# Kernel optimization log

Hardware: AMD Instinct MI355X
Metric: run time of the kernel (lower is better)

Reference implementation:

```python
import jax, jax.numpy as jnp
import numpy as np

N = 50000      # nodes
E = 1600000    # edges
IN = 128       # in_feats
H = 4          # heads
F = 32         # per-head feats (h_feats = out_feats = 32)
NEG_SLOPE = 0.2


def setup_inputs() -> dict:
    key = jax.random.key(0)
    ks = jax.random.split(key, 12)
    glorot = lambda k, shape: jax.random.normal(k, shape, jnp.float32) * np.sqrt(2.0 / (shape[0] + shape[-1])).astype(np.float32)
    x = jax.random.normal(ks[0], (N, IN), jnp.float32)
    edge_index = jax.random.randint(ks[1], (2, E), 0, N, dtype=jnp.int32)
    W1 = glorot(ks[2], (IN, H * F))
    att_src1 = glorot(ks[3], (H, F))
    att_dst1 = glorot(ks[4], (H, F))
    b1 = jnp.zeros((F,), jnp.float32)
    W2 = glorot(ks[5], (F, H * F))
    att_src2 = glorot(ks[6], (H, F))
    att_dst2 = glorot(ks[7], (H, F))
    b2 = jnp.zeros((F,), jnp.float32)
    return {"x": x, "edge_index": edge_index,
            "W1": W1, "att_src1": att_src1, "att_dst1": att_dst1, "b1": b1,
            "W2": W2, "att_src2": att_src2, "att_dst2": att_dst2, "b2": b2}


def gat_conv(x, edge_index, W, a_src, a_dst, bias):
    """PyG GATConv with concat=False (head-average), add_self_loops=True."""
    n = x.shape[0]
    h = (x @ W).reshape(n, H, F)                      # [N,H,F]
    loops = jnp.arange(n, dtype=edge_index.dtype)
    src = jnp.concatenate([edge_index[0], loops])     # [E+N]
    dst = jnp.concatenate([edge_index[1], loops])
    alpha_src = jnp.einsum('nhf,hf->nh', h, a_src)    # [N,H]
    alpha_dst = jnp.einsum('nhf,hf->nh', h, a_dst)
    e = jax.nn.leaky_relu(alpha_src[src] + alpha_dst[dst], NEG_SLOPE)  # [E+N,H]
    # scatter-softmax over incoming edges per destination node
    m = jax.ops.segment_max(e, dst, num_segments=n)
    e = jnp.exp(e - m[dst])
    s = jax.ops.segment_sum(e, dst, num_segments=n)
    alpha = e / (s[dst] + 1e-16)                      # [E+N,H]
    out = jax.ops.segment_sum(alpha[:, :, None] * h[src], dst, num_segments=n)  # [N,H,F]
    return out.mean(axis=1) + bias                    # concat=False: average heads


def reference(x, edge_index, W1, att_src1, att_dst1, b1, W2, att_src2, att_dst2, b2):
    h = gat_conv(x, edge_index, W1, att_src1, att_dst1, b1)
    h = jax.nn.elu(h)
    return gat_conv(h, edge_index, W2, att_src2, att_dst2, b2)
```

## Files before the change

### kernel.cpp

```cpp
#include <hip/hip_runtime.h>
#include <hip/hip_bf16.h>
#include <hip/hip_fp16.h>
#include <math.h>


#define NS 64
#define NB 4
#define MAXNPB 12500

__device__ __forceinline__ float lrelu(float x) { return x > 0.f ? x : 0.2f * x; }

__device__ __forceinline__ unsigned int fenc(float f) {
    unsigned int u = __float_as_uint(f);
    return (u & 0x80000000u) ? ~u : (u | 0x80000000u);
}
__device__ __forceinline__ float fdec(unsigned int e) {
    unsigned int u = (e & 0x80000000u) ? (e & 0x7FFFFFFFu) : ~e;
    return __uint_as_float(u);
}

__device__ __forceinline__ unsigned short f2bf(float x) {
    unsigned u = __float_as_uint(x);
    return (unsigned short)((u + 0x7FFFu + ((u >> 16) & 1u)) >> 16);
}
__device__ __forceinline__ float bflo(unsigned w) { return __uint_as_float(w << 16); }
__device__ __forceinline__ float bfhi(unsigned w) { return __uint_as_float(w & 0xFFFF0000u); }

__device__ __forceinline__ unsigned pack_h2(float a, float b) {
    const __half2 h = __float22half2_rn(make_float2(a, b));
    return *(const unsigned*)&h;
}
__device__ __forceinline__ float2 unpack_h2(unsigned w) {
    __half2 h = *(const __half2*)&w;
    return __half22float2(h);
}

__global__ __launch_bounds__(512) void hist_kernel(
    const int* __restrict__ dst, unsigned short* __restrict__ cnt_priv,
    int E, int n, int npb) {
    __shared__ int h[MAXNPB];
    const int b = blockIdx.x & (NB - 1);
    const int s = blockIdx.x / NB;
    const int lo = b * npb;
    const int hi = min(lo + npb, n);
    const int span = hi - lo;
    if (span <= 0) return;
    for (int j = threadIdx.x; j < span; j += 512) h[j] = 0;
    __syncthreads();
    const int E4 = E >> 2;
    const int len4 = (E4 + NS - 1) / NS;
    const int beg4 = s * len4;
    const int end4 = min(beg4 + len4, E4);
    const int4* dst4 = (const int4*)dst;
    for (int i = beg4 + threadIdx.x; i < end4; i += 512) {
        const int4 d = dst4[i];
        if (d.x >= lo && d.x < hi) atomicAdd(&h[d.x - lo], 1);
        if (d.y >= lo && d.y < hi) atomicAdd(&h[d.y - lo], 1);
        if (d.z >= lo && d.z < hi) atomicAdd(&h[d.z - lo], 1);
        if (d.w >= lo && d.w < hi) atomicAdd(&h[d.w - lo], 1);
    }
    if (s == NS - 1) {
        for (int i = (E4 << 2) + threadIdx.x; i < E; i += 512) {
            const int d = dst[i];
            if (d >= lo && d < hi) atomicAdd(&h[d - lo], 1);
        }
    }
    __syncthreads();
    unsigned short* outp = cnt_priv + (size_t)s * n + lo;
    for (int j = threadIdx.x; j < span; j += 512) outp[j] = (unsigned short)h[j];
}

__global__ __launch_bounds__(256) void scan_part(unsigned short* __restrict__ cnt_priv,
                                                 int* __restrict__ deg,
                                                 int* __restrict__ bsum, int n) {
    __shared__ int red[256];
    const int t = threadIdx.x;
    const int node = blockIdx.x * 256 + t;
    int run = 0;
    if (node < n) {
#pragma unroll 4
        for (int s = 0; s < NS; ++s) {
            unsigned short* p = &cnt_priv[(size_t)s * n + node];
            const int c = *p;
            *p = (unsigned short)run;
            run += c;
        }
        deg[node] = run;
    }
    red[t] = (node < n) ? run : 0;
    __syncthreads();
    for (int o = 128; o > 0; o >>= 1) {
        if (t < o) red[t] += red[t + o];
        __syncthreads();
    }
    if (t == 0) bsum[blockIdx.x] = red[0];
}

__global__ __launch_bounds__(256) void scan_mid(const int* __restrict__ bsum,
                                                int* __restrict__ boff, int nb,
                                                int* __restrict__ rowptr, int n) {
    __shared__ int s[256];
    const int t = threadIdx.x;
    const int v = (t < nb) ? bsum[t] : 0;
    s[t] = v;
    __syncthreads();
    for (int o = 1; o < 256; o <<= 1) {
        const int u = (t >= o) ? s[t - o] : 0;
        __syncthreads();
        s[t] += u;
        __syncthreads();
    }
    if (t < nb) boff[t] = s[t] - v;
    if (t == 255) rowptr[n] = s[255];
}

__global__ __launch_bounds__(256) void scan_final(const int* __restrict__ deg,
                                                  const int* __restrict__ boff,
                                                  int* __restrict__ rowptr, int n) {
    __shared__ int s[256];
    const int t = threadIdx.x;
    const int i = blockIdx.x * 256 + t;
    const int v = (i < n) ? deg[i] : 0;
    s[t] = v;
    __syncthreads();
    for (int o = 1; o < 256; o <<= 1) {
        const int u = (t >= o) ? s[t - o] : 0;
        __syncthreads();
        s[t] += u;
        __syncthreads();
    }
    if (i < n) rowptr[i] = boff[blockIdx.x] + s[t] - v;
}

__global__ __launch_bounds__(512) void scatter_kernel(
    const int* __restrict__ src, const int* __restrict__ dst,
    const int* __restrict__ rowptr, const unsigned short* __restrict__ cnt_priv,
    const float* __restrict__ asrc, const float* __restrict__ adst,
    const unsigned int* __restrict__ gmax,
    uint4* __restrict__ esd, int E, int n, int npb) {
    __shared__ int cur[MAXNPB];
    const int b = blockIdx.x & (NB - 1);
    const int s = blockIdx.x / NB;
    const int lo = b * npb;
    const int hi = min(lo + npb, n);
    const int span = hi - lo;
    if (span <= 0) return;
    {
        const unsigned short* cp = cnt_priv + (size_t)s * n + lo;
        const int* rp = rowptr + lo;
        for (int j = threadIdx.x; j < span; j += 512) cur[j] = rp[j] + (int)cp[j];
    }
    __syncthreads();
    const char* aB = (const char*)asrc;
    const char* dB = (const char*)adst;
    const float g0 = fdec(gmax[0]), g1 = fdec(gmax[1]);
    const float g2 = fdec(gmax[2]), g3 = fdec(gmax[3]);

    auto place = [&](int sv, int dv) {
        const int p = atomicAdd(&cur[dv - lo], 1);
        const unsigned s16 = (unsigned)(sv << 4);
        const unsigned d16 = (unsigned)(dv << 4);
        const float4 as = *(const float4*)(aB + s16);
        const float4 ad = *(const float4*)(dB + d16);
        const float q0 = __expf(lrelu(as.x + ad.x) - lrelu(g0 + ad.x));
        const float q1 = __expf(lrelu(as.y + ad.y) - lrelu(g1 + ad.y));
        const float q2 = __expf(lrelu(as.z + ad.z) - lrelu(g2 + ad.z));
        const float q3 = __expf(lrelu(as.w + ad.w) - lrelu(g3 + ad.w));
        esd[p] = make_uint4(s16, d16, pack_h2(q0, q1), pack_h2(q2, q3));
    };

    const int E4 = E >> 2;
    const int len4 = (E4 + NS - 1) / NS;
    const int beg4 = s * len4;
    const int end4 = min(beg4 + len4, E4);
    const int4* dst4 = (const int4*)dst;
    const int4* src4 = (const int4*)src;
    for (int i = beg4 + threadIdx.x; i < end4; i += 512) {
        const int4 d = dst4[i];
        const int4 sv = src4[i];
        if (d.x >= lo && d.x < hi) place(sv.x, d.x);
        if (d.y >= lo && d.y < hi) place(sv.y, d.y);
        if (d.z >= lo && d.z < hi) place(sv.z, d.z);
        if (d.w >= lo && d.w < hi) place(sv.w, d.w);
    }
    if (s == NS - 1) {
        for (int i = (E4 << 2) + threadIdx.x; i < E; i += 512) {
            const int d = dst[i];
            if (d >= lo && d < hi) place(src[i], d);
        }
    }
}

__global__ __launch_bounds__(256) void edge_w_kernel(
    uint4* __restrict__ esd,
    const float* __restrict__ asrc, const float* __restrict__ adst,
    const unsigned int* __restrict__ gmax, int Etot) {
    const char* aB = (const char*)asrc;
    const char* dB = (const char*)adst;
    const float g0 = fdec(gmax[0]), g1 = fdec(gmax[1]);
    const float g2 = fdec(gmax[2]), g3 = fdec(gmax[3]);
    for (int i = blockIdx.x * blockDim.x + threadIdx.x; i < Etot;
         i += gridDim.x * blockDim.x) {
        const unsigned long long sd =
            __builtin_nontemporal_load((const unsigned long long*)&esd[i]);
        const unsigned s16 = (unsigned)sd;
        const unsigned d16 = (unsigned)(sd >> 32);
        const float4 as = *(const float4*)(aB + s16);
        const float4 ad = *(const float4*)(dB + d16);
        const float q0 = __expf(lrelu(as.x + ad.x) - lrelu(g0 + ad.x));
        const float q1 = __expf(lrelu(as.y + ad.y) - lrelu(g1 + ad.y));
        const float q2 = __expf(lrelu(as.z + ad.z) - lrelu(g2 + ad.z));
        const float q3 = __expf(lrelu(as.w + ad.w) - lrelu(g3 + ad.w));
        const unsigned long long rec =
            ((unsigned long long)pack_h2(q2, q3) << 32) | pack_h2(q0, q1);
        __builtin_nontemporal_store(
            rec, (unsigned long long*)((char*)&esd[i] + 8));
    }
}

template <int K>
__global__ __launch_bounds__(256) void gemm_kernel(
    const float* __restrict__ X, const float* __restrict__ W,
    const float* __restrict__ AttS, const float* __restrict__ AttD,
    unsigned short* __restrict__ Hb, float* __restrict__ asrc, float* __restrict__ adst,
    unsigned int* __restrict__ gmax, int n) {
    constexpr int KC = 32;
    __shared__ __align__(16) float Ws[KC * 128];
    __shared__ __align__(16) float Xs[64 * K];
    __shared__ unsigned int smax[4];
    const int tid = threadIdx.x;

    const int r = tid >> 5;
    const int sub = tid & 31;
    const int head = sub >> 3;
    const int pos = ((head & 1) << 1) | (head >> 1);
    const int fc = (sub & 7) * 4;
    const int rowBase = blockIdx.x * 64;

    if (tid < 4) smax[tid] = 0u;
    {
        const float4* X4 = (const float4*)X;
        float4* Xs4 = (float4*)Xs;
        const int K4 = K / 4;
        for (int i = tid; i < 64 * K4; i += 256) {
            int rr = rowBase + i / K4;
            Xs4[i] = (rr < n) ? X4[(size_t)rr * K4 + (i % K4)] : make_float4(0.f, 0.f, 0.f, 0.f);
        }
    }

    float acc[8][4] = {};
    const float4* Ws4 = (const float4*)Ws;
    for (int kt = 0; kt < K; kt += KC) {
        __syncthreads();
        {
            const float4* W4 = (const float4*)(W + kt * 128);
            float4* WsS = (float4*)Ws;
#pragma unroll
            for (int i = 0; i < 4; ++i) WsS[tid + i * 256] = W4[tid + i * 256];
        }
        __syncthreads();
#pragma unroll
        for (int k = 0; k < KC; k += 4) {
            float4 wv[4];
#pragma unroll
            for (int j = 0; j < 4; ++j) wv[j] = Ws4[(k + j) * 32 + sub];
            float4 xv[8];
#pragma unroll
            for (int b = 0; b < 8; ++b)
                xv[b] = *(const float4*)&Xs[(b * 8 + r) * K + kt + k];
#pragma unroll
            for (int b = 0; b < 8; ++b) {
                acc[b][0] = fmaf(xv[b].x, wv[0].x, acc[b][0]);
                acc[b][1] = fmaf(xv[b].x, wv[0].y, acc[b][1]);
                acc[b][2] = fmaf(xv[b].x, wv[0].z, acc[b][2]);
                acc[b][3] = fmaf(xv[b].x, wv[0].w, acc[b][3]);
                acc[b][0] = fmaf(xv[b].y, wv[1].x, acc[b][0]);
                acc[b][1] = fmaf(xv[b].y, wv[1].y, acc[b][1]);
                acc[b][2] = fmaf(xv[b].y, wv[1].z, acc[b][2]);
                acc[b][3] = fmaf(xv[b].y, wv[1].w, acc[b][3]);
                acc[b][0] = fmaf(xv[b].z, wv[2].x, acc[b][0]);
                acc[b][1] = fmaf(xv[b].z, wv[2].y, acc[b][1]);
                acc[b][2] = fmaf(xv[b].z, wv[2].z, acc[b][2]);
                acc[b][3] = fmaf(xv[b].z, wv[2].w, acc[b][3]);
                acc[b][0] = fmaf(xv[b].w, wv[3].x, acc[b][0]);
                acc[b][1] = fmaf(xv[b].w, wv[3].y, acc[b][1]);
                acc[b][2] = fmaf(xv[b].w, wv[3].z, acc[b][2]);
                acc[b][3] = fmaf(xv[b].w, wv[3].w, acc[b][3]);
            }
        }
    }

    float a_s[4], a_d[4];
#pragma unroll
    for (int j = 0; j < 4; ++j) {
        a_s[j] = AttS[head * 32 + fc + j];
        a_d[j] = AttD[head * 32 + fc + j];
    }
#pragma unroll
    for (int b = 0; b < 8; ++b) {
        const int row = rowBase + b * 8 + r;
        const float p0 = __shfl_xor(acc[b][0], 16);
        const float p1 = __shfl_xor(acc[b][1], 16);
        const float p2 = __shfl_xor(acc[b][2], 16);
        const float p3 = __shfl_xor(acc[b][3], 16);
        if (row < n) {
            if (head < 2) {
                char* base = (char*)Hb + (size_t)row * 256 + (unsigned)fc * 8 + head * 4;
                *(unsigned*)(base + 0)  = (unsigned)f2bf(acc[b][0]) | ((unsigned)f2bf(p0) << 16);
                *(unsigned*)(base + 8)  = (unsigned)f2bf(acc[b][1]) | ((unsigned)f2bf(p1) << 16);
                *(unsigned*)(base + 16) = (unsigned)f2bf(acc[b][2]) | ((unsigned)f2bf(p2) << 16);
                *(unsigned*)(base + 24) = (unsigned)f2bf(acc[b][3]) | ((unsigned)f2bf(p3) << 16);
            }
            float ps = acc[b][0] * a_s[0] + acc[b][1] * a_s[1] +
                       acc[b][2] * a_s[2] + acc[b][3] * a_s[3];
            float pd = acc[b][0] * a_d[0] + acc[b][1] * a_d[1] +
                       acc[b][2] * a_d[2] + acc[b][3] * a_d[3];
#pragma unroll
            for (int msk = 1; msk < 8; msk <<= 1) {
                ps += __shfl_xor(ps, msk);
                pd += __shfl_xor(pd, msk);
            }
            if ((sub & 7) == 0) {
                asrc[row * 4 + pos] = ps;
                adst[row * 4 + pos] = pd;
                atomicMax(&smax[pos], fenc(ps));
            }
        }
    }
    __syncthreads();
    if (tid < 4) atomicMax(&gmax[tid], smax[tid]);
}

__global__ __launch_bounds__(256) void node_kernel(
    const int* __restrict__ rowptr, const uint4* __restrict__ esd,
    const unsigned short* __restrict__ Hb, const float* __restrict__ asrc,
    const float* __restrict__ adst, const unsigned int* __restrict__ gmax,
    const float* __restrict__ bias,
    float* __restrict__ outp, int n, int apply_elu) {
    const int node = blockIdx.x * 8 + (threadIdx.x >> 5);
    if (node >= n) return;
    const unsigned f = threadIdx.x & 31;
    const unsigned f8 = f * 8;
    const char* hB = (const char*)Hb;
    const unsigned long long* eB = (const unsigned long long*)esd;

    const int beg = rowptr[node], end = rowptr[node + 1];
    const float4 ad4 = *(const float4*)(adst + (size_t)node * 4);
    const float4 as4 = *(const float4*)(asrc + (size_t)node * 4);
    const float M0 = lrelu(fdec(gmax[0]) + ad4.x);
    const float M1 = lrelu(fdec(gmax[1]) + ad4.y);
    const float M2 = lrelu(fdec(gmax[2]) + ad4.z);
    const float M3 = lrelu(fdec(gmax[3]) + ad4.w);

    const float q0 = __expf(lrelu(as4.x + ad4.x) - M0);
    const float q1 = __expf(lrelu(as4.y + ad4.y) - M1);
    const float q2 = __expf(lrelu(as4.z + ad4.z) - M2);
    const float q3 = __expf(lrelu(as4.w + ad4.w) - M3);
    float s0 = q0, s1 = q1, s2 = q2, s3 = q3;
    const uint2 hs = *(const uint2*)(hB + ((size_t)node << 8) + f8);
    float a0 = q0 * bflo(hs.x);
    float a1 = q1 * bfhi(hs.x);
    float a2 = q2 * bflo(hs.y);
    float a3 = q3 * bfhi(hs.y);

    int i = beg;
    for (; i + 8 <= end; i += 8) {
        unsigned long long e0[8], e1[8];
#pragma unroll
        for (int u = 0; u < 8; ++u) {
            e0[u] = __builtin_nontemporal_load(&eB[(size_t)(i + u) * 2]);
            e1[u] = __builtin_nontemporal_load(&eB[(size_t)(i + u) * 2 + 1]);
        }
        uint2 h[8];
#pragma unroll
        for (int u = 0; u < 8; ++u)
            h[u] = *(const uint2*)(hB + (((unsigned)e0[u]) << 4) + f8);
#pragma unroll
        for (int u = 0; u < 8; ++u) {
            const float2 qa = unpack_h2((unsigned)e1[u]);
            const float2 qb = unpack_h2((unsigned)(e1[u] >> 32));
            s0 += qa.x; s1 += qa.y; s2 += qb.x; s3 += qb.y;
            a0 = fmaf(qa.x, bflo(h[u].x), a0);
            a1 = fmaf(qa.y, bfhi(h[u].x), a1);
            a2 = fmaf(qb.x, bflo(h[u].y), a2);
            a3 = fmaf(qb.y, bfhi(h[u].y), a3);
        }
    }
    for (; i < end; ++i) {
        const unsigned long long e0 = __builtin_nontemporal_load(&eB[(size_t)i * 2]);
        const unsigned long long e1 = __builtin_nontemporal_load(&eB[(size_t)i * 2 + 1]);
        const uint2 h = *(const uint2*)(hB + (((unsigned)e0) << 4) + f8);
        const float2 qa = unpack_h2((unsigned)e1);
        const float2 qb = unpack_h2((unsigned)(e1 >> 32));
        s0 += qa.x; s1 += qa.y; s2 += qb.x; s3 += qb.y;
        a0 = fmaf(qa.x, bflo(h.x), a0);
        a1 = fmaf(qa.y, bfhi(h.x), a1);
        a2 = fmaf(qb.x, bflo(h.y), a2);
        a3 = fmaf(qb.y, bfhi(h.y), a3);
    }

    float v = a0 / s0 + a1 / s1 + a2 / s2 + a3 / s3;
    v = v * 0.25f + bias[f];
    if (apply_elu) v = (v > 0.f) ? v : (__expf(v) - 1.f);
    outp[(size_t)node * 32 + f] = v;
}


extern "C" void kernel_launch(void* const* d_in, const int* in_sizes, int n_in,
                              void* d_out, int out_size, void* d_ws, size_t ws_size,
                              hipStream_t stream) {
    const int N = in_sizes[0] / 128;
    const int E = in_sizes[1] / 2;
    const float* x = (const float*)d_in[0];
    const int* ei = (const int*)d_in[1];
    const float* W1 = (const float*)d_in[2];
    const float* atS1 = (const float*)d_in[3];
    const float* atD1 = (const float*)d_in[4];
    const float* b1 = (const float*)d_in[5];
    const float* W2 = (const float*)d_in[6];
    const float* atS2 = (const float*)d_in[7];
    const float* atD2 = (const float*)d_in[8];
    const float* b2 = (const float*)d_in[9];
    float* out = (float*)d_out;

    char* ws = (char*)d_ws;
    size_t off = 0;
    auto alloc = [&](size_t bytes) {
        void* p = ws + off;
        off = (off + bytes + 255) & ~(size_t)255;
        return p;
    };
    unsigned int* gmax = (unsigned int*)alloc(8 * sizeof(unsigned int));
    unsigned short* cnt_priv = (unsigned short*)alloc((size_t)NS * N * 2);
    int* deg = (int*)alloc((size_t)N * 4);
    int* rowptr = (int*)alloc((size_t)(N + 1) * 4);
    int* bsum = (int*)alloc(256 * 4);
    int* boff = (int*)alloc(256 * 4);
    uint4* esd = (uint4*)alloc((size_t)E * 16);
    unsigned short* hb = (unsigned short*)alloc((size_t)N * 128 * 2);
    float* av_s = (float*)alloc((size_t)N * 4 * 4);
    float* av_d = (float*)alloc((size_t)N * 4 * 4);
    float* x2 = (float*)alloc((size_t)N * 32 * 4);

    const int* e_src = ei;
    const int* e_dst = ei + E;

    const int gemmGrid = (N + 63) / 64;
    const int nodeGrid = (N + 7) / 8;
    const int npb = (N + NB - 1) / NB;
    const int scanGrid = (N + 255) / 256;
    const int bsGrid = NB * NS;

    (void)hipMemsetAsync(gmax, 0, 8 * sizeof(unsigned int), stream);

    hist_kernel<<<bsGrid, 512, 0, stream>>>(e_dst, cnt_priv, E, N, npb);
    scan_part<<<scanGrid, 256, 0, stream>>>(cnt_priv, deg, bsum, N);
    scan_mid<<<1, 256, 0, stream>>>(bsum, boff, scanGrid, rowptr, N);
    scan_final<<<scanGrid, 256, 0, stream>>>(deg, boff, rowptr, N);

    gemm_kernel<128><<<gemmGrid, 256, 0, stream>>>(
        x, W1, atS1, atD1, hb, av_s, av_d, gmax, N);
    scatter_kernel<<<bsGrid, 512, 0, stream>>>(
        e_src, e_dst, rowptr, cnt_priv, av_s, av_d, gmax, esd, E, N, npb);
    node_kernel<<<nodeGrid, 256, 0, stream>>>(rowptr, esd, hb, av_s, av_d, gmax,
                                              b1, x2, N, 1);
    gemm_kernel<32><<<gemmGrid, 256, 0, stream>>>(
        x2, W2, atS2, atD2, hb, av_s, av_d, gmax + 4, N);
    edge_w_kernel<<<2048, 256, 0, stream>>>(esd, av_s, av_d, gmax + 4, E);
    node_kernel<<<nodeGrid, 256, 0, stream>>>(rowptr, esd, hb, av_s, av_d, gmax + 4,
                                              b2, out, N, 0);
}
```

Measured before the change: 330.3 us.

## Fuse destination histogram into first GEMM launch and deepen node-kernel unroll

The destination-degree histogram blocks now run as extra blocks of the layer-1 GEMM launch, sharing one shared-memory buffer, so the independent histogram and GEMM work overlap and one launch is removed. Histogram blocks use 256 threads instead of 512. The node aggregation loop is unrolled to 16 edges with a 4-edge tail to put more gathers in flight, at the cost of more registers. The shared buffer sized to the larger of the two uses may reduce GEMM occupancy.

```diff
diff --git a/kernel.cpp b/kernel.cpp
--- a/kernel.cpp
+++ b/kernel.cpp
@@ -33,41 +33,6 @@
 __device__ __forceinline__ float2 unpack_h2(unsigned w) {
     __half2 h = *(const __half2*)&w;
     return __half22float2(h);
-}
-
-__global__ __launch_bounds__(512) void hist_kernel(
-    const int* __restrict__ dst, unsigned short* __restrict__ cnt_priv,
-    int E, int n, int npb) {
-    __shared__ int h[MAXNPB];
-    const int b = blockIdx.x & (NB - 1);
-    const int s = blockIdx.x / NB;
-    const int lo = b * npb;
-    const int hi = min(lo + npb, n);
-    const int span = hi - lo;
-    if (span <= 0) return;
-    for (int j = threadIdx.x; j < span; j += 512) h[j] = 0;
-    __syncthreads();
-    const int E4 = E >> 2;
-    const int len4 = (E4 + NS - 1) / NS;
-    const int beg4 = s * len4;
-    const int end4 = min(beg4 + len4, E4);
-    const int4* dst4 = (const int4*)dst;
-    for (int i = beg4 + threadIdx.x; i < end4; i += 512) {
-        const int4 d = dst4[i];
-        if (d.x >= lo && d.x < hi) atomicAdd(&h[d.x - lo], 1);
-        if (d.y >= lo && d.y < hi) atomicAdd(&h[d.y - lo], 1);
-        if (d.z >= lo && d.z < hi) atomicAdd(&h[d.z - lo], 1);
-        if (d.w >= lo && d.w < hi) atomicAdd(&h[d.w - lo], 1);
-    }
-    if (s == NS - 1) {
-        for (int i = (E4 << 2) + threadIdx.x; i < E; i += 512) {
-            const int d = dst[i];
-            if (d >= lo && d < hi) atomicAdd(&h[d - lo], 1);
-        }
-    }
-    __syncthreads();
-    unsigned short* outp = cnt_priv + (size_t)s * n + lo;
-    for (int j = threadIdx.x; j < span; j += 512) outp[j] = (unsigned short)h[j];
 }
 
 __global__ __launch_bounds__(256) void scan_part(unsigned short* __restrict__ cnt_priv,
@@ -219,17 +184,60 @@
 }
 
 template <int K>
-__global__ __launch_bounds__(256) void gemm_kernel(
+__global__ __launch_bounds__(256) void gemm_hist(
     const float* __restrict__ X, const float* __restrict__ W,
     const float* __restrict__ AttS, const float* __restrict__ AttD,
     unsigned short* __restrict__ Hb, float* __restrict__ asrc, float* __restrict__ adst,
-    unsigned int* __restrict__ gmax, int n) {
+    unsigned int* __restrict__ gmax, int n, int gemmGrid,
+    const int* __restrict__ dst, unsigned short* __restrict__ cnt_priv,
+    int E, int npb) {
     constexpr int KC = 32;
-    __shared__ __align__(16) float Ws[KC * 128];
-    __shared__ __align__(16) float Xs[64 * K];
+    constexpr int GEMM_BYTES = KC * 128 * 4 + 64 * K * 4;
+    constexpr int HIST_BYTES = (K == 128) ? (MAXNPB * 4) : 0;
+    constexpr int SMEM_BYTES = (GEMM_BYTES > HIST_BYTES) ? GEMM_BYTES : HIST_BYTES;
+    __shared__ __align__(16) char smem[SMEM_BYTES];
     __shared__ unsigned int smax[4];
     const int tid = threadIdx.x;
 
+    if constexpr (K == 128) {
+        if (blockIdx.x >= gemmGrid) {
+            int* h = (int*)smem;
+            const int hb = blockIdx.x - gemmGrid;
+            const int b = hb & (NB - 1);
+            const int s = hb / NB;
+            const int lo = b * npb;
+            const int hi = min(lo + npb, n);
+            const int span = hi - lo;
+            if (span <= 0) return;
+            for (int j = tid; j < span; j += 256) h[j] = 0;
+            __syncthreads();
+            const int E4 = E >> 2;
+            const int len4 = (E4 + NS - 1) / NS;
+            const int beg4 = s * len4;
+            const int end4 = min(beg4 + len4, E4);
+            const int4* dst4 = (const int4*)dst;
+            for (int i = beg4 + tid; i < end4; i += 256) {
+                const int4 d = dst4[i];
+                if (d.x >= lo && d.x < hi) atomicAdd(&h[d.x - lo], 1);
+                if (d.y >= lo && d.y < hi) atomicAdd(&h[d.y - lo], 1);
+                if (d.z >= lo && d.z < hi) atomicAdd(&h[d.z - lo], 1);
+                if (d.w >= lo && d.w < hi) atomicAdd(&h[d.w - lo], 1);
+            }
+            if (s == NS - 1) {
+                for (int i = (E4 << 2) + tid; i < E; i += 256) {
+                    const int d = dst[i];
+                    if (d >= lo && d < hi) atomicAdd(&h[d - lo], 1);
+                }
+            }
+            __syncthreads();
+            unsigned short* outp = cnt_priv + (size_t)s * n + lo;
+            for (int j = tid; j < span; j += 256) outp[j] = (unsigned short)h[j];
+            return;
+        }
+    }
+
+    float* Ws = (float*)smem;
+    float* Xs = (float*)(smem + KC * 128 * 4);
     const int r = tid >> 5;
     const int sub = tid & 31;
     const int head = sub >> 3;
@@ -364,19 +372,41 @@
     float a3 = q3 * bfhi(hs.y);
 
     int i = beg;
-    for (; i + 8 <= end; i += 8) {
-        unsigned long long e0[8], e1[8];
-#pragma unroll
-        for (int u = 0; u < 8; ++u) {
+    for (; i + 16 <= end; i += 16) {
+        unsigned long long e0[16], e1[16];
+#pragma unroll
+        for (int u = 0; u < 16; ++u) {
             e0[u] = __builtin_nontemporal_load(&eB[(size_t)(i + u) * 2]);
             e1[u] = __builtin_nontemporal_load(&eB[(size_t)(i + u) * 2 + 1]);
         }
-        uint2 h[8];
-#pragma unroll
-        for (int u = 0; u < 8; ++u)
+        uint2 h[16];
+#pragma unroll
+        for (int u = 0; u < 16; ++u)
             h[u] = *(const uint2*)(hB + (((unsigned)e0[u]) << 4) + f8);
 #pragma unroll
-        for (int u = 0; u < 8; ++u) {
+        for (int u = 0; u < 16; ++u) {
+            const float2 qa = unpack_h2((unsigned)e1[u]);
+            const float2 qb = unpack_h2((unsigned)(e1[u] >> 32));
+            s0 += qa.x; s1 += qa.y; s2 += qb.x; s3 += qb.y;
+            a0 = fmaf(qa.x, bflo(h[u].x), a0);
+            a1 = fmaf(qa.y, bfhi(h[u].x), a1);
+            a2 = fmaf(qb.x, bflo(h[u].y), a2);
+            a3 = fmaf(qb.y, bfhi(h[u].y), a3);
+        }
+    }
+    for (; i + 4 <= end; i += 4) {
+        unsigned long long e0[4], e1[4];
+#pragma unroll
+        for (int u = 0; u < 4; ++u) {
+            e0[u] = __builtin_nontemporal_load(&eB[(size_t)(i + u) * 2]);
+            e1[u] = __builtin_nontemporal_load(&eB[(size_t)(i + u) * 2 + 1]);
+        }
+        uint2 h[4];
+#pragma unroll
+        for (int u = 0; u < 4; ++u)
+            h[u] = *(const uint2*)(hB + (((unsigned)e0[u]) << 4) + f8);
+#pragma unroll
+        for (int u = 0; u < 4; ++u) {
             const float2 qa = unpack_h2((unsigned)e1[u]);
             const float2 qb = unpack_h2((unsigned)(e1[u] >> 32));
             s0 += qa.x; s1 += qa.y; s2 += qb.x; s3 += qb.y;
@@ -453,19 +483,19 @@
 
     (void)hipMemsetAsync(gmax, 0, 8 * sizeof(unsigned int), stream);
 
-    hist_kernel<<<bsGrid, 512, 0, stream>>>(e_dst, cnt_priv, E, N, npb);
+    gemm_hist<128><<<gemmGrid + bsGrid, 256, 0, stream>>>(
+        x, W1, atS1, atD1, hb, av_s, av_d, gmax, N, gemmGrid,
+        e_dst, cnt_priv, E, npb);
     scan_part<<<scanGrid, 256, 0, stream>>>(cnt_priv, deg, bsum, N);
     scan_mid<<<1, 256, 0, stream>>>(bsum, boff, scanGrid, rowptr, N);
     scan_final<<<scanGrid, 256, 0, stream>>>(deg, boff, rowptr, N);
-
-    gemm_kernel<128><<<gemmGrid, 256, 0, stream>>>(
-        x, W1, atS1, atD1, hb, av_s, av_d, gmax, N);
     scatter_kernel<<<bsGrid, 512, 0, stream>>>(
         e_src, e_dst, rowptr, cnt_priv, av_s, av_d, gmax, esd, E, N, npb);
     node_kernel<<<nodeGrid, 256, 0, stream>>>(rowptr, esd, hb, av_s, av_d, gmax,
                                               b1, x2, N, 1);
-    gemm_kernel<32><<<gemmGrid, 256, 0, stream>>>(
-        x2, W2, atS2, atD2, hb, av_s, av_d, gmax + 4, N);
+    gemm_hist<32><<<gemmGrid, 256, 0, stream>>>(
+        x2, W2, atS2, atD2, hb, av_s, av_d, gmax + 4, N, gemmGrid,
+        nullptr, nullptr, 0, 0);
     edge_w_kernel<<<2048, 256, 0, stream>>>(esd, av_s, av_d, gmax + 4, E);
     node_kernel<<<nodeGrid, 256, 0, stream>>>(rowptr, esd, hb, av_s, av_d, gmax + 4,
                                               b2, out, N, 0);
```

Result: no change. 335.0 us (+1.4%).
